# Kernel optimization log

Measured on AMD Instinct MI355X. Metric: run time of the kernel, lower is better.

The kernel has to match this reference:

```python
import jax, jax.numpy as jnp
from jax import lax
import numpy as np

N, I, O = 64, 8, 8
B = 512
S_EX, S_PHI, S_RHO = 10, 60, 60  # S_phi must equal S_rho (alpha loops feed S_rho-sized h into the GRUs)
N_ACTIONS, N_ROLES = 5, 7


def _gru(x, h, Wih, Whh, bih, bhh):
    # torch.nn.GRUCell math
    gi = x @ Wih.T + bih
    gh = h @ Whh.T + bhh
    ir, iz, inn = jnp.split(gi, 3, axis=-1)
    hr, hz, hn = jnp.split(gh, 3, axis=-1)
    r = jax.nn.sigmoid(ir + hr)
    zg = jax.nn.sigmoid(iz + hz)
    n = jnp.tanh(inn + r * hn)
    return (1.0 - zg) * n + zg * h


def setup_inputs() -> dict:
    key = jax.random.key(0)
    ks = jax.random.split(key, 24)
    f32 = jnp.float32
    z = jax.random.normal(ks[0], (B, N, S_EX), f32)
    dz = jax.random.normal(ks[1], (B, N, S_EX), f32)
    has = (jax.random.uniform(ks[2], (B, N)) < 0.9).astype(f32)
    adj = (jnp.triu(jax.random.uniform(ks[3], (N, N)), 1) > 0.7).astype(jnp.int32)

    def lin(k, o, i):
        return (jax.random.normal(k, (o, i), f32) * np.float32(1.0 / np.sqrt(i)))

    d = dict(z=z, dz=dz, has=has, adj=adj)
    d['Wih_f'] = lin(ks[4], 3 * S_PHI, S_RHO)
    d['Whh_f'] = lin(ks[5], 3 * S_PHI, S_PHI)
    d['bih_f'] = jax.random.normal(ks[6], (3 * S_PHI,), f32) * 0.02
    d['bhh_f'] = jax.random.normal(ks[7], (3 * S_PHI,), f32) * 0.02
    d['Wih_b'] = lin(ks[8], 3 * S_PHI, S_RHO)
    d['Whh_b'] = lin(ks[9], 3 * S_PHI, S_PHI)
    d['bih_b'] = jax.random.normal(ks[10], (3 * S_PHI,), f32) * 0.02
    d['bhh_b'] = jax.random.normal(ks[11], (3 * S_PHI,), f32) * 0.02
    d['Wf'] = lin(ks[12], S_RHO, S_PHI + 2 * S_EX)
    d['bf'] = jax.random.normal(ks[13], (S_RHO,), f32) * 0.02
    d['Wb'] = lin(ks[14], S_RHO, S_PHI + 2 * S_EX)
    d['bb'] = jax.random.normal(ks[15], (S_RHO,), f32) * 0.02
    d['Wa'] = lin(ks[16], N_ACTIONS, 2 * S_PHI)
    d['ba'] = jax.random.normal(ks[17], (N_ACTIONS,), f32) * 0.02
    d['Wc'] = lin(ks[18], 1, 2 * S_PHI)
    d['bc'] = jax.random.normal(ks[19], (1,), f32) * 0.02
    d['Wu'] = lin(ks[20], N_ROLES, 2 * S_RHO)
    d['bu'] = jax.random.normal(ks[21], (N_ROLES,), f32) * 0.02
    return d


def reference(z, dz, has, adj,
              Wih_f, Whh_f, bih_f, bhh_f,
              Wih_b, Whh_b, bih_b, bhh_b,
              Wf, bf, Wb, bb, Wa, ba, Wc, bc, Wu, bu):
    Bn, Nn = has.shape
    dt = z.dtype
    adjf = adj.astype(dt)

    # ---- forward sweep over nodes in ascending order ----
    def fwd_outer(rho, i):
        def inner(h, j):
            hn = _gru(rho[j], h, Wih_f, Whh_f, bih_f, bhh_f)
            blend = adjf[j, i] * has[:, j][:, None]  # edge exists AND source node present
            return h + blend * (hn - h), None
        h, _ = lax.scan(inner, jnp.zeros((Bn, S_PHI), dt), jnp.arange(Nn))
        rho_i = jnp.tanh(jnp.concatenate([h, z[:, i], dz[:, i]], 1) @ Wf.T + bf)
        return rho.at[i].set(rho_i), None

    rho_f, _ = lax.scan(fwd_outer, jnp.zeros((Nn, Bn, S_RHO), dt), jnp.arange(Nn))

    # ---- backward sweep over nodes in descending order ----
    def bwd_outer(rho, i):
        def inner(h, j):
            hn = _gru(rho[j], h, Wih_b, Whh_b, bih_b, bhh_b)
            blend = adjf[i, j] * has[:, j][:, None]  # out-edges of i, visited descending
            return h + blend * (hn - h), None
        h, _ = lax.scan(inner, jnp.zeros((Bn, S_PHI), dt), jnp.arange(Nn - 1, -1, -1))
        rho_i = jnp.concatenate([h, z[:, i], dz[:, i]], 1) @ Wb.T + bb
        return rho.at[i].set(rho_i), None

    rho_b, _ = lax.scan(bwd_outer, jnp.zeros((Nn, Bn, S_RHO), dt), jnp.arange(Nn - 1, -1, -1))

    # ---- aggregate outputs (last O nodes) and inputs (first I nodes) ----
    h = jnp.zeros((Bn, S_RHO), dt)
    for i in range(N - O, N):
        hn = _gru(rho_f[i], h, Wih_f, Whh_f, bih_f, bhh_f)
        h = h + has[:, i][:, None] * (hn - h)
    alpha_f = h
    h = jnp.zeros((Bn, S_RHO), dt)
    for i in reversed(range(I)):
        hn = _gru(rho_b[i], h, Wih_b, Whh_b, bih_b, bhh_b)
        h = h + has[:, i][:, None] * (hn - h)
    alpha_b = h

    ab = jnp.concatenate([alpha_f, alpha_b], 1)
    omega = ab @ Wa.T + ba          # [B, 5]
    value = ab @ Wc.T + bc          # [B, 1]

    feats = jnp.concatenate([rho_f, rho_b], -1)           # [N, B, 2*S_rho]
    psi = jnp.einsum('nbs,rs->brn', feats, Wu) + bu[None, :, None]  # [B, 7, N]
    m = has[:, None, :]
    psi = -60.0 * (1.0 - m) + psi * m  # interpolate(-60, psi, has)

    instr_prob = jax.nn.softmax(omega, axis=1)
    role_prob = jax.nn.softmax(psi, axis=2)
    return instr_prob, role_prob, value
```

## Files before the change

kernel.cpp:

```cpp
#include <hip/hip_runtime.h>
#include <hip/hip_bf16.h>

#define NN 64
#define BATCH 512
#define SP 60
#define SG 180
#define SEX 10
#define CATD 80
#define NA 5
#define NR 7
#define OO 8
#define II 8

typedef unsigned long long u64;
typedef unsigned short u16;
typedef unsigned int u32;
typedef unsigned char u8;

#define OFF_Z     0
#define OFF_DZ    327680
#define OFF_HAS   655360
#define OFF_WIHF  688128
#define OFF_WHHF  698928
#define OFF_BIHF  709728
#define OFF_BHHF  709908
#define OFF_WIHB  710088
#define OFF_WHHB  720888
#define OFF_BIHB  731688
#define OFF_BHHB  731868
#define OFF_WF    732048
#define OFF_BF    736848
#define OFF_WB    736908
#define OFF_BB    741708
#define OFF_WA    741768
#define OFF_BA    742368
#define OFF_WC    742373
#define OFF_BC    742493
#define OFF_WU    742494
#define OFF_BU    743334
#define CONV_TOTAL 743341
#define OFF_FLAG  743342
#define OFF_RHOF  743344
#define OFF_RHOB  (OFF_RHOF + 1966080)
#define OFF_ALF   (OFF_RHOB + 1966080)
#define OFF_ALB   (OFF_ALF + 30720)
#define OUT_TOTAL 232448

typedef _Float16 f16;
typedef _Float16 half2_t __attribute__((ext_vector_type(2)));
typedef _Float16 f16x8 __attribute__((ext_vector_type(8)));
typedef float f32x4 __attribute__((ext_vector_type(4)));

__device__ __forceinline__ float us2f(u16 v){
  return __uint_as_float(((u32)v) << 16);
}
__device__ __forceinline__ u16 f2bf(float f){
  __hip_bfloat16 h = __float2bfloat16(f);
  return *reinterpret_cast<u16*>(&h);
}
__device__ __forceinline__ float rcp_(float x){ return __builtin_amdgcn_rcpf(x); }
__device__ __forceinline__ float sigm(float x){
  return rcp_(1.f + __expf(-x));
}
__device__ __forceinline__ float tanh_(float x){
  float e = __expf(2.f*fabsf(x));
  float t = 1.f - 2.f*rcp_(e + 1.f);
  return copysignf(t, x);
}
__device__ __forceinline__ u32 pack2(float a, float b){
  half2_t h; h[0] = (f16)a; h[1] = (f16)b;
  return __builtin_bit_cast(u32, h);
}
__device__ __forceinline__ float fdot2_(u32 a, u32 b, float c){
  return __builtin_amdgcn_fdot2(__builtin_bit_cast(half2_t, a),
                                __builtin_bit_cast(half2_t, b), c, false);
}
__device__ __forceinline__ f16x8 bc16(uint4 v){ return __builtin_bit_cast(f16x8, v); }
__device__ __forceinline__ f32x4 mfma16(f16x8 a, f16x8 b, f32x4 c){
  return __builtin_amdgcn_mfma_f32_16x16x32_f16(a, b, c, 0, 0, 0);
}

__global__ __launch_bounds__(256) void conv_in(
  const void* z, const void* dz, const void* has,
  const void* WihF, const void* WhhF, const void* bihF, const void* bhhF,
  const void* WihB, const void* WhhB, const void* bihB, const void* bhhB,
  const void* Wf_, const void* bf_, const void* Wb_, const void* bb_,
  const void* Wa, const void* ba, const void* Wc, const void* bc,
  const void* Wu, const void* bu, float* ws)
{
  __shared__ int sIsBf;
  const int tid = threadIdx.x;
  if (tid < 64){
    const u32* w = (const u32*)has;
    int f = 0;
    #pragma unroll
    for (int k=0;k<4;k++) f |= (w[tid*4 + k] == 0x3F803F80u) ? 1 : 0;
    u64 m = __ballot(f != 0);
    if (tid == 0) sIsBf = (m != 0ULL) ? 1 : 0;
  }
  __syncthreads();
  const int isbf = sIsBf;
  if (blockIdx.x == 0 && tid == 0) ws[OFF_FLAG] = (float)isbf;
  int idx = blockIdx.x*256 + tid;
  if (idx >= CONV_TOTAL) return;
  const void* src; int loc;
  if      (idx < OFF_DZ  ){ src=z;    loc=idx-OFF_Z;    }
  else if (idx < OFF_HAS ){ src=dz;   loc=idx-OFF_DZ;   }
  else if (idx < OFF_WIHF){ src=has;  loc=idx-OFF_HAS;  }
  else if (idx < OFF_WHHF){ src=WihF; loc=idx-OFF_WIHF; }
  else if (idx < OFF_BIHF){ src=WhhF; loc=idx-OFF_WHHF; }
  else if (idx < OFF_BHHF){ src=bihF; loc=idx-OFF_BIHF; }
  else if (idx < OFF_WIHB){ src=bhhF; loc=idx-OFF_BHHF; }
  else if (idx < OFF_WHHB){ src=WihB; loc=idx-OFF_WIHB; }
  else if (idx < OFF_BIHB){ src=WhhB; loc=idx-OFF_WHHB; }
  else if (idx < OFF_BHHB){ src=bihB; loc=idx-OFF_BIHB; }
  else if (idx < OFF_WF  ){ src=bhhB; loc=idx-OFF_BHHB; }
  else if (idx < OFF_BF  ){ src=Wf_;  loc=idx-OFF_WF;   }
  else if (idx < OFF_WB  ){ src=bf_;  loc=idx-OFF_BF;   }
  else if (idx < OFF_BB  ){ src=Wb_;  loc=idx-OFF_WB;   }
  else if (idx < OFF_WA  ){ src=bb_;  loc=idx-OFF_BB;   }
  else if (idx < OFF_BA  ){ src=Wa;   loc=idx-OFF_WA;   }
  else if (idx < OFF_WC  ){ src=ba;   loc=idx-OFF_BA;   }
  else if (idx < OFF_BC  ){ src=Wc;   loc=idx-OFF_WC;   }
  else if (idx < OFF_WU  ){ src=bc;   loc=idx-OFF_BC;   }
  else if (idx < OFF_BU  ){ src=Wu;   loc=idx-OFF_WU;   }
  else                    { src=bu;   loc=idx-OFF_BU;   }
  float v = isbf ? us2f(((const u16*)src)[loc]) : ((const float*)src)[loc];
  ws[idx] = v;
}

__global__ __launch_bounds__(256, 4) void dir_kernel(const int* __restrict__ adj,
                                                     float* __restrict__ ws)
{
  const int tid = threadIdx.x;
  const int w   = tid >> 6;
  const int u   = tid & 63;
  const int ml  = u & 15;
  const int q   = u >> 4;
  const int bid = blockIdx.x;
  const int bwd = bid >> 9;
  const int b   = bid & 511;

  const float* Wih  = ws + (bwd ? OFF_WIHB : OFF_WIHF);
  const float* Whh  = ws + (bwd ? OFF_WHHB : OFF_WHHF);
  const float* bih  = ws + (bwd ? OFF_BIHB : OFF_BIHF);
  const float* bhh  = ws + (bwd ? OFF_BHHB : OFF_BHHF);
  const float* Wcat = ws + (bwd ? OFF_WB   : OFF_WF);
  const float* bcat = ws + (bwd ? OFF_BB   : OFF_BF);
  const float* zc   = ws + OFF_Z;
  const float* dzc  = ws + OFF_DZ;
  const float* hasc = ws + OFF_HAS;
  float* rho   = ws + (bwd ? OFF_RHOB : OFF_RHOF);
  float* alpha = ws + (bwd ? OFF_ALB  : OFF_ALF);

  __shared__ uint4 sH4[65][9];
  __shared__ uint4 sRhoPad[8];
  __shared__ uint4 sRhoHist[8][8];
  __shared__ float sZdc[NN][64];
  __shared__ u32 sZp[NN][5];
  __shared__ u32 sDZp[NN][5];
  __shared__ float sHas[NN];
  __shared__ u64 sRowM[NN];
  __shared__ u8 sConsL[NN][64];
  __shared__ int sConsCnt[NN];

  #define ROWB(I) ((char*)&sH4[(I)][0])
  const u32 BIASW = 0x3C000000u;

  {
    if (tid < 64){
      u64 rowm = 0;
      for (int j=0;j<64;j++) rowm |= ((u64)(adj[tid*64+j]!=0))<<j;
      sRowM[tid] = rowm;
      sHas[tid] = hasc[b*NN + tid];
    }
    for (int idx=tid; idx<65*9; idx+=256){
      uint4 v = {0,0,0,0};
      if (idx % 9 == 7) v.w = BIASW;
      ((uint4*)sH4)[idx] = v;
    }
    if (tid < 8){ uint4 v={0,0,0,0}; if (tid==7) v.w = BIASW; sRhoPad[tid]=v; }
    if (tid < 64){ uint4 v={0,0,0,0}; if ((tid&7)==7) v.w = BIASW; ((uint4*)sRhoHist)[tid]=v; }
    for (int idx=tid; idx<NN*5; idx+=256){
      int n2=idx/5, p2=idx%5;
      sZp [n2][p2] = pack2(zc [(size_t)b*NN*SEX + n2*SEX + 2*p2],
                           zc [(size_t)b*NN*SEX + n2*SEX + 2*p2+1]);
      sDZp[n2][p2] = pack2(dzc[(size_t)b*NN*SEX + n2*SEX + 2*p2],
                           dzc[(size_t)b*NN*SEX + n2*SEX + 2*p2+1]);
    }
  }
  __syncthreads();
  if (tid < 64){
    u64 cm = 0;
    if (bwd) for (int i2=0;i2<64;i2++) cm |= ((sRowM[i2]>>tid)&1ULL)<<i2;
    u64 m = bwd ? cm : sRowM[tid];
    int c = 0;
    while (m){ int i2 = (int)__builtin_ctzll(m); m &= m-1; sConsL[tid][c++] = (u8)i2; }
    sConsCnt[tid] = c;
  }
  {
    const int uu = tid & 63;
    const int tw = tid >> 6;
    if (uu < SP){
      u32 wz[10];
      #pragma unroll
      for (int p=0;p<10;p++)
        wz[p] = pack2(Wcat[uu*CATD + 60 + 2*p], Wcat[uu*CATD + 60 + 2*p + 1]);
      const float bb0 = bcat[uu];
      for (int t2=tw; t2<NN; t2+=4){
        float c = bb0;
        #pragma unroll
        for (int p=0;p<5;p++){
          c = fdot2_(wz[p],   sZp [t2][p], c);
          c = fdot2_(wz[5+p], sDZp[t2][p], c);
        }
        sZdc[t2][uu] = c;
      }
    }
  }

  f16x8 Ar[4], Az[4], Anh[2], Ani[2], Ac[2];
  {
    const int R = 16*w + ml;
    const bool rok = (R < SP);
    #pragma unroll
    for (int kt=0; kt<4; kt++){
      f16x8 vr, vz;
      #pragma unroll
      for (int j=0;j<8;j++){
        const int K = 32*kt + 8*q + j;
        float wr=0.f, wz2=0.f;
        if (rok){
          if (K < SP){ wr = Whh[R*SP+K]; wz2 = Whh[(60+R)*SP+K]; }
          else if (K >= 64 && K < 64+SP){ wr = Wih[R*SP+(K-64)]; wz2 = Wih[(60+R)*SP+(K-64)]; }
          else if (K == 127){ wr = bhh[R]+bih[R]; wz2 = bhh[60+R]+bih[60+R]; }
        }
        vr[j]=(f16)wr; vz[j]=(f16)wz2;
      }
      Ar[kt]=vr; Az[kt]=vz;
    }
    #pragma unroll
    for (int kt=0; kt<2; kt++){
      f16x8 vn, vi, vc;
      #pragma unroll
      for (int j=0;j<8;j++){
        const int K = 32*kt + 8*q + j;
        float wn=0.f, wi=0.f, wcv=0.f;
        if (rok){
          if (K < SP){ wn = Whh[(120+R)*SP+K]; wi = Wih[(120+R)*SP+K]; wcv = Wcat[R*CATD+K]; }
          else if (K == 63){ wn = bhh[120+R]; wi = bih[120+R]; }
        }
        vn[j]=(f16)wn; vi[j]=(f16)wi; vc[j]=(f16)wcv;
      }
      Anh[kt]=vn; Ani[kt]=vi; Ac[kt]=vc;
    }
  }
  __syncthreads();

  auto gates = [&](f32x4 Dr, f32x4 Dz, f32x4 Dn, f32x4 Gn,
                   int ci, bool wr, float bl){
    char* rp = ROWB(ci) + 32*w + 8*q;
    uint2 h2 = *(uint2*)rp;
    half2_t ha = __builtin_bit_cast(half2_t, h2.x);
    half2_t hb = __builtin_bit_cast(half2_t, h2.y);
    float hold[4] = { (float)ha[0], (float)ha[1], (float)hb[0], (float)hb[1] };
    float hw[4];
    #pragma unroll
    for (int reg=0;reg<4;reg++){
      float r_ = sigm(Dr[reg]);
      float zg = sigm(Dz[reg]);
      float nv = tanh_(Gn[reg] + r_*Dn[reg]);
      float hn_ = (1.f - zg)*nv + zg*hold[reg];
      hw[reg] = (bl != 0.f) ? hn_ : hold[reg];
    }
    if (wr && !(w==3 && q==3)){
      uint2 o; o.x = pack2(hw[0],hw[1]); o.y = pack2(hw[2],hw[3]);
      *(uint2*)rp = o;
    }
  };

  auto fullpass = [&](f16x8 Bh0, f16x8 Bh1, f16x8 Br0, f16x8 Br1,
                      f32x4 Gn, int ci, bool wr, float bl){
    f32x4 Dr={0,0,0,0}, Dz={0,0,0,0}, Dn={0,0,0,0};
    Dr = mfma16(Ar[0], Bh0, Dr); Dr = mfma16(Ar[1], Bh1, Dr);
    Dr = mfma16(Ar[2], Br0, Dr); Dr = mfma16(Ar[3], Br1, Dr);
    Dz = mfma16(Az[0], Bh0, Dz); Dz = mfma16(Az[1], Bh1, Dz);
    Dz = mfma16(Az[2], Br0, Dz); Dz = mfma16(Az[3], Br1, Dz);
    Dn = mfma16(Anh[0], Bh0, Dn); Dn = mfma16(Anh[1], Bh1, Dn);
    gates(Dr, Dz, Dn, Gn, ci, wr, bl);
  };

  int t = bwd ? 63 : 0;
  const int dt = bwd ? -1 : 1;
  for (int s=0; s<64; s++, t+=dt){
    const float blendT = sHas[t];
    const int cnt = sConsCnt[t];
    const bool act = (blendT != 0.f) && (cnt > 0);
    const bool g1  = act && (cnt > 16);

    int ci0 = 64, ci1 = 64;
    f16x8 Bh0g0={}, Bh1g0={}, Bh0g1={}, Bh1g1={};
    if (act){
      ci0 = (ml < cnt) ? (int)sConsL[t][ml] : 64;
      Bh0g0 = bc16(sH4[ci0][q]);
      Bh1g0 = bc16(sH4[ci0][4+q]);
      if (g1){
        ci1 = (16 + ml < cnt) ? (int)sConsL[t][16 + ml] : 64;
        Bh0g1 = bc16(sH4[ci1][q]);
        Bh1g1 = bc16(sH4[ci1][4+q]);
      }
    }

    {
      const f16x8 Hb0 = bc16(sH4[t][q]);
      const f16x8 Hb1 = bc16(sH4[t][4+q]);
      f32x4 Rv = {0,0,0,0};
      Rv = mfma16(Ac[0], Hb0, Rv);
      Rv = mfma16(Ac[1], Hb1, Rv);
      const int row = 16*w + 4*q + ml;
      if (ml < 4 && row < SP){
        float vv = Rv[0];
        vv = (ml==1) ? Rv[1] : vv;
        vv = (ml==2) ? Rv[2] : vv;
        vv = (ml==3) ? Rv[3] : vv;
        vv += sZdc[t][row];
        if (!bwd) vv = tanh_(vv);
        *(f16*)((char*)&sRhoPad[0] + 2*row) = (f16)vv;
        const int slot = bwd ? t : (t - (NN-OO));
        if (slot >= 0 && slot < 8)
          *(f16*)((char*)&sRhoHist[slot][0] + 2*row) = (f16)vv;
        rho[((size_t)t*BATCH + b)*SP + row] = vv;
      }
    }
    __syncthreads();

    if (act){
      const f16x8 Br0 = bc16(sRhoPad[q]);
      const f16x8 Br1 = bc16(sRhoPad[4+q]);
      f32x4 Gn={0,0,0,0};
      Gn = mfma16(Ani[0], Br0, Gn); Gn = mfma16(Ani[1], Br1, Gn);
      f32x4 Pr={0,0,0,0};
      Pr = mfma16(Ar[2], Br0, Pr); Pr = mfma16(Ar[3], Br1, Pr);
      f32x4 Pz={0,0,0,0};
      Pz = mfma16(Az[2], Br0, Pz); Pz = mfma16(Az[3], Br1, Pz);

      {
        f32x4 Dr=Pr, Dz=Pz, Dn={0,0,0,0};
        Dr = mfma16(Ar[0], Bh0g0, Dr); Dr = mfma16(Ar[1], Bh1g0, Dr);
        Dz = mfma16(Az[0], Bh0g0, Dz); Dz = mfma16(Az[1], Bh1g0, Dz);
        Dn = mfma16(Anh[0], Bh0g0, Dn); Dn = mfma16(Anh[1], Bh1g0, Dn);
        gates(Dr, Dz, Dn, Gn, ci0, ml < cnt, 1.0f);
      }
      if (g1){
        f32x4 Dr=Pr, Dz=Pz, Dn={0,0,0,0};
        Dr = mfma16(Ar[0], Bh0g1, Dr); Dr = mfma16(Ar[1], Bh1g1, Dr);
        Dz = mfma16(Az[0], Bh0g1, Dz); Dz = mfma16(Az[1], Bh1g1, Dz);
        Dn = mfma16(Anh[0], Bh0g1, Dn); Dn = mfma16(Anh[1], Bh1g1, Dn);
        gates(Dr, Dz, Dn, Gn, ci1, 16 + ml < cnt, 1.0f);
      }
      for (int p=2; 16*p < cnt; p++){
        const int idxp = 16*p + ml;
        const int ci = (idxp < cnt) ? (int)sConsL[t][idxp] : 64;
        const f16x8 Bh0 = bc16(sH4[ci][q]);
        const f16x8 Bh1 = bc16(sH4[ci][4+q]);
        fullpass(Bh0, Bh1, Br0, Br1, Gn, ci, idxp < cnt, 1.0f);
      }
    }
    __syncthreads();
  }

  for (int s2=0; s2<8; s2++){
    const int i = bwd ? (7 - s2) : (NN - OO + s2);
    const int slot = bwd ? i : (i - (NN-OO));
    const f16x8 Th0 = bc16(sH4[64][q]);
    const f16x8 Th1 = bc16(sH4[64][4+q]);
    const f16x8 Tr0 = bc16(sRhoHist[slot][q]);
    const f16x8 Tr1 = bc16(sRhoHist[slot][4+q]);
    f32x4 Gt={0,0,0,0};
    Gt = mfma16(Ani[0], Tr0, Gt);
    Gt = mfma16(Ani[1], Tr1, Gt);
    __syncthreads();
    fullpass(Th0, Th1, Tr0, Tr1, Gt, 64, ml==0, sHas[i]);
    __syncthreads();
  }
  if (tid < SP) alpha[(size_t)b*SP + tid] = (float)*(const f16*)(ROWB(64) + 2*tid);
  #undef ROWB
}

__global__ __launch_bounds__(256, 1) void head_kernel(float* __restrict__ ws,
                                                      void* __restrict__ outp)
{
  const int b = blockIdx.x;
  const int tid = threadIdx.x;
  const int isbf = (ws[OFF_FLAG] != 0.f);
  const float* hasc   = ws + OFF_HAS;
  const float* WaC    = ws + OFF_WA;
  const float* baC    = ws + OFF_BA;
  const float* WcC    = ws + OFF_WC;
  const float* bcC    = ws + OFF_BC;
  const float* WuC    = ws + OFF_WU;
  const float* buC    = ws + OFF_BU;
  const float* rhoF   = ws + OFF_RHOF;
  const float* rhoB   = ws + OFF_RHOB;
  const float* alphaF = ws + OFF_ALF;
  const float* alphaB = ws + OFF_ALB;

  __shared__ float sF[NN][122];
  __shared__ float sAB[120];
  __shared__ float sWu[NR*120];
  __shared__ float sHasR[NN];
  __shared__ float sPsi[NR][NN];
  __shared__ float sOm[NA];

  auto wout = [&](int idx, float v){
    if (isbf) ((u16*)outp)[idx] = f2bf(v);
    else      ((float*)outp)[idx] = v;
  };

  for (int idx=tid; idx<NN*SP; idx+=256){
    int n = idx/SP, s = idx%SP;
    sF[n][s]    = rhoF[((size_t)n*BATCH + b)*SP + s];
    sF[n][60+s] = rhoB[((size_t)n*BATCH + b)*SP + s];
  }
  for (int idx=tid; idx<120; idx+=256)
    sAB[idx] = (idx<60) ? alphaF[(size_t)b*SP + idx] : alphaB[(size_t)b*SP + idx-60];
  for (int idx=tid; idx<NR*120; idx+=256) sWu[idx] = WuC[idx];
  for (int idx=tid; idx<NN; idx+=256) sHasR[idx] = hasc[b*NN + idx];
  __syncthreads();

  for (int idx=tid; idx<NR*NN; idx+=256){
    int r = idx/NN, n = idx%NN;
    const float2* fn = (const float2*)&sF[n][0];
    const float2* wr = (const float2*)&sWu[r*120];
    float acc = buC[r];
    #pragma unroll 6
    for (int s2=0;s2<60;s2++){
      float2 a = fn[s2], c = wr[s2];
      acc += a.x*c.x;
      acc += a.y*c.y;
    }
    sPsi[r][n] = (sHasR[n] != 0.f) ? acc : -60.f;
  }
  if (tid >= 64 && tid < 64+NA){
    int a = tid - 64;
    float acc = baC[a];
    for (int s=0;s<120;s++) acc += sAB[s]*WaC[a*120+s];
    sOm[a] = acc;
  }
  if (tid == 70){
    float acc = bcC[0];
    for (int s=0;s<120;s++) acc += sAB[s]*WcC[s];
    wout(2560 + BATCH*NR*NN + b, acc);
  }
  __syncthreads();

  if (tid < NR*32){
    const int r = tid >> 5, l = tid & 31;
    float v0 = sPsi[r][l], v1 = sPsi[r][l+32];
    float m = fmaxf(v0, v1);
    #pragma unroll
    for (int o=16;o>0;o>>=1) m = fmaxf(m, __shfl_xor(m, o, 64));
    float e0 = __expf(v0 - m), e1 = __expf(v1 - m);
    float ssum = e0 + e1;
    #pragma unroll
    for (int o=16;o>0;o>>=1) ssum += __shfl_xor(ssum, o, 64);
    float rinv = 1.f/ssum;
    wout(2560 + (size_t)b*NR*NN + r*NN + l,    e0*rinv);
    wout(2560 + (size_t)b*NR*NN + r*NN + l+32, e1*rinv);
  }
  if (tid == 224){
    float m = -1e30f;
    for (int a=0;a<NA;a++) m = fmaxf(m, sOm[a]);
    float e[NA]; float ssum = 0.f;
    for (int a=0;a<NA;a++){ e[a] = __expf(sOm[a]-m); ssum += e[a]; }
    for (int a=0;a<NA;a++) wout(b*NA + a, e[a]/ssum);
  }
}

extern "C" void kernel_launch(void* const* d_in, const int* in_sizes, int n_in,
                              void* d_out, int out_size, void* d_ws, size_t ws_size,
                              hipStream_t stream)
{
  const int* adj = (const int*)d_in[3];
  float* ws = (float*)d_ws;

  conv_in<<<(CONV_TOTAL+255)/256, 256, 0, stream>>>(
      d_in[0], d_in[1], d_in[2],
      d_in[4], d_in[5], d_in[6], d_in[7],
      d_in[8], d_in[9], d_in[10], d_in[11],
      d_in[12], d_in[13], d_in[14], d_in[15],
      d_in[16], d_in[17], d_in[18], d_in[19],
      d_in[20], d_in[21], ws);

  dir_kernel<<<1024, 256, 0, stream>>>(adj, ws);

  head_kernel<<<512, 256, 0, stream>>>(ws, d_out);
}
```

Baseline: 256.9 us.

## Process two batch elements per workgroup in the directional GRU kernel

Each workgroup of the directional DAG-GRU kernel now handles two batch elements instead of one, halving the grid to 512 blocks. The two independent MFMA chains are interleaved so that register-resident weight fragments, the adjacency and consumer-list setup, and the per-step barriers are shared between them. The blend is now a per-element has mask applied in the gate update rather than a per-step skip. In exchange, register pressure and shared memory per block roughly double, the launch bound drops to 2 blocks per CU, and steps where only one element is present still do the work for both.

```diff
diff --git a/kernel.cpp b/kernel.cpp
--- a/kernel.cpp
+++ b/kernel.cpp
@@ -129,7 +129,7 @@
   ws[idx] = v;
 }
 
-__global__ __launch_bounds__(256, 4) void dir_kernel(const int* __restrict__ adj,
+__global__ __launch_bounds__(256, 2) void dir_kernel(const int* __restrict__ adj,
                                                      float* __restrict__ ws)
 {
   const int tid = threadIdx.x;
@@ -138,8 +138,8 @@
   const int ml  = u & 15;
   const int q   = u >> 4;
   const int bid = blockIdx.x;
-  const int bwd = bid >> 9;
-  const int b   = bid & 511;
+  const int bwd = bid >> 8;
+  const int bp  = (bid & 255) << 1;
 
   const float* Wih  = ws + (bwd ? OFF_WIHB : OFF_WIHF);
   const float* Whh  = ws + (bwd ? OFF_WHHB : OFF_WHHF);
@@ -153,18 +153,18 @@
   float* rho   = ws + (bwd ? OFF_RHOB : OFF_RHOF);
   float* alpha = ws + (bwd ? OFF_ALB  : OFF_ALF);
 
-  __shared__ uint4 sH4[65][9];
-  __shared__ uint4 sRhoPad[8];
-  __shared__ uint4 sRhoHist[8][8];
-  __shared__ float sZdc[NN][64];
-  __shared__ u32 sZp[NN][5];
-  __shared__ u32 sDZp[NN][5];
-  __shared__ float sHas[NN];
+  __shared__ uint4 sH4[2][65][9];
+  __shared__ uint4 sRhoPad[2][8];
+  __shared__ uint4 sRhoHist[2][8][8];
+  __shared__ float sZdc[2][NN][SP];
+  __shared__ u32 sZp[2][NN][5];
+  __shared__ u32 sDZp[2][NN][5];
+  __shared__ float sHas[2][NN];
   __shared__ u64 sRowM[NN];
   __shared__ u8 sConsL[NN][64];
   __shared__ int sConsCnt[NN];
 
-  #define ROWB(I) ((char*)&sH4[(I)][0])
+  #define ROWB(E,I) ((char*)&sH4[(E)][(I)][0])
   const u32 BIASW = 0x3C000000u;
 
   {
@@ -172,21 +172,24 @@
       u64 rowm = 0;
       for (int j=0;j<64;j++) rowm |= ((u64)(adj[tid*64+j]!=0))<<j;
       sRowM[tid] = rowm;
-      sHas[tid] = hasc[b*NN + tid];
-    }
-    for (int idx=tid; idx<65*9; idx+=256){
+    }
+    if (tid < 128){
+      const int e = tid >> 6, n = tid & 63;
+      sHas[e][n] = hasc[(bp+e)*NN + n];
+    }
+    for (int idx=tid; idx<2*65*9; idx+=256){
       uint4 v = {0,0,0,0};
-      if (idx % 9 == 7) v.w = BIASW;
+      if ((idx % 9) == 7) v.w = BIASW;
       ((uint4*)sH4)[idx] = v;
     }
-    if (tid < 8){ uint4 v={0,0,0,0}; if (tid==7) v.w = BIASW; sRhoPad[tid]=v; }
-    if (tid < 64){ uint4 v={0,0,0,0}; if ((tid&7)==7) v.w = BIASW; ((uint4*)sRhoHist)[tid]=v; }
-    for (int idx=tid; idx<NN*5; idx+=256){
-      int n2=idx/5, p2=idx%5;
-      sZp [n2][p2] = pack2(zc [(size_t)b*NN*SEX + n2*SEX + 2*p2],
-                           zc [(size_t)b*NN*SEX + n2*SEX + 2*p2+1]);
-      sDZp[n2][p2] = pack2(dzc[(size_t)b*NN*SEX + n2*SEX + 2*p2],
-                           dzc[(size_t)b*NN*SEX + n2*SEX + 2*p2+1]);
+    if (tid < 16){ uint4 v={0,0,0,0}; if ((tid&7)==7) v.w = BIASW; ((uint4*)sRhoPad)[tid]=v; }
+    if (tid < 128){ uint4 v={0,0,0,0}; if ((tid&7)==7) v.w = BIASW; ((uint4*)sRhoHist)[tid]=v; }
+    for (int idx=tid; idx<2*NN*5; idx+=256){
+      int e = idx/(NN*5), rem = idx%(NN*5), n2=rem/5, p2=rem%5;
+      sZp [e][n2][p2] = pack2(zc [(size_t)(bp+e)*NN*SEX + n2*SEX + 2*p2],
+                              zc [(size_t)(bp+e)*NN*SEX + n2*SEX + 2*p2+1]);
+      sDZp[e][n2][p2] = pack2(dzc[(size_t)(bp+e)*NN*SEX + n2*SEX + 2*p2],
+                              dzc[(size_t)(bp+e)*NN*SEX + n2*SEX + 2*p2+1]);
     }
   }
   __syncthreads();
@@ -207,14 +210,15 @@
       for (int p=0;p<10;p++)
         wz[p] = pack2(Wcat[uu*CATD + 60 + 2*p], Wcat[uu*CATD + 60 + 2*p + 1]);
       const float bb0 = bcat[uu];
-      for (int t2=tw; t2<NN; t2+=4){
+      for (int et=tw; et<2*NN; et+=4){
+        const int e = et >> 6, t2 = et & 63;
         float c = bb0;
         #pragma unroll
         for (int p=0;p<5;p++){
-          c = fdot2_(wz[p],   sZp [t2][p], c);
-          c = fdot2_(wz[5+p], sDZp[t2][p], c);
+          c = fdot2_(wz[p],   sZp [e][t2][p], c);
+          c = fdot2_(wz[5+p], sDZp[e][t2][p], c);
         }
-        sZdc[t2][uu] = c;
+        sZdc[e][t2][uu] = c;
       }
     }
   }
@@ -258,8 +262,8 @@
   __syncthreads();
 
   auto gates = [&](f32x4 Dr, f32x4 Dz, f32x4 Dn, f32x4 Gn,
-                   int ci, bool wr, float bl){
-    char* rp = ROWB(ci) + 32*w + 8*q;
+                   char* rowb, bool wr, float bl){
+    char* rp = rowb + 32*w + 8*q;
     uint2 h2 = *(uint2*)rp;
     half2_t ha = __builtin_bit_cast(half2_t, h2.x);
     half2_t hb = __builtin_bit_cast(half2_t, h2.y);
@@ -280,90 +284,117 @@
   };
 
   auto fullpass = [&](f16x8 Bh0, f16x8 Bh1, f16x8 Br0, f16x8 Br1,
-                      f32x4 Gn, int ci, bool wr, float bl){
+                      f32x4 Gn, char* rowb, bool wr, float bl){
     f32x4 Dr={0,0,0,0}, Dz={0,0,0,0}, Dn={0,0,0,0};
     Dr = mfma16(Ar[0], Bh0, Dr); Dr = mfma16(Ar[1], Bh1, Dr);
     Dr = mfma16(Ar[2], Br0, Dr); Dr = mfma16(Ar[3], Br1, Dr);
     Dz = mfma16(Az[0], Bh0, Dz); Dz = mfma16(Az[1], Bh1, Dz);
     Dz = mfma16(Az[2], Br0, Dz); Dz = mfma16(Az[3], Br1, Dz);
     Dn = mfma16(Anh[0], Bh0, Dn); Dn = mfma16(Anh[1], Bh1, Dn);
-    gates(Dr, Dz, Dn, Gn, ci, wr, bl);
+    gates(Dr, Dz, Dn, Gn, rowb, wr, bl);
   };
 
   int t = bwd ? 63 : 0;
   const int dt = bwd ? -1 : 1;
   for (int s=0; s<64; s++, t+=dt){
-    const float blendT = sHas[t];
     const int cnt = sConsCnt[t];
-    const bool act = (blendT != 0.f) && (cnt > 0);
+    const float bl0 = sHas[0][t];
+    const float bl1 = sHas[1][t];
+    const bool act = (cnt > 0) && (bl0 != 0.f || bl1 != 0.f);
     const bool g1  = act && (cnt > 16);
 
     int ci0 = 64, ci1 = 64;
-    f16x8 Bh0g0={}, Bh1g0={}, Bh0g1={}, Bh1g1={};
+    f16x8 Bh0e0={}, Bh1e0={}, Bh0e1={}, Bh1e1={};
+    f16x8 Ch0e0={}, Ch1e0={}, Ch0e1={}, Ch1e1={};
     if (act){
       ci0 = (ml < cnt) ? (int)sConsL[t][ml] : 64;
-      Bh0g0 = bc16(sH4[ci0][q]);
-      Bh1g0 = bc16(sH4[ci0][4+q]);
+      Bh0e0 = bc16(sH4[0][ci0][q]); Bh1e0 = bc16(sH4[0][ci0][4+q]);
+      Bh0e1 = bc16(sH4[1][ci0][q]); Bh1e1 = bc16(sH4[1][ci0][4+q]);
       if (g1){
         ci1 = (16 + ml < cnt) ? (int)sConsL[t][16 + ml] : 64;
-        Bh0g1 = bc16(sH4[ci1][q]);
-        Bh1g1 = bc16(sH4[ci1][4+q]);
+        Ch0e0 = bc16(sH4[0][ci1][q]); Ch1e0 = bc16(sH4[0][ci1][4+q]);
+        Ch0e1 = bc16(sH4[1][ci1][q]); Ch1e1 = bc16(sH4[1][ci1][4+q]);
       }
     }
 
     {
-      const f16x8 Hb0 = bc16(sH4[t][q]);
-      const f16x8 Hb1 = bc16(sH4[t][4+q]);
-      f32x4 Rv = {0,0,0,0};
-      Rv = mfma16(Ac[0], Hb0, Rv);
-      Rv = mfma16(Ac[1], Hb1, Rv);
+      const f16x8 H00 = bc16(sH4[0][t][q]);
+      const f16x8 H01 = bc16(sH4[0][t][4+q]);
+      const f16x8 H10 = bc16(sH4[1][t][q]);
+      const f16x8 H11 = bc16(sH4[1][t][4+q]);
+      f32x4 Rv0 = {0,0,0,0}, Rv1 = {0,0,0,0};
+      Rv0 = mfma16(Ac[0], H00, Rv0);
+      Rv1 = mfma16(Ac[0], H10, Rv1);
+      Rv0 = mfma16(Ac[1], H01, Rv0);
+      Rv1 = mfma16(Ac[1], H11, Rv1);
       const int row = 16*w + 4*q + ml;
       if (ml < 4 && row < SP){
-        float vv = Rv[0];
-        vv = (ml==1) ? Rv[1] : vv;
-        vv = (ml==2) ? Rv[2] : vv;
-        vv = (ml==3) ? Rv[3] : vv;
-        vv += sZdc[t][row];
-        if (!bwd) vv = tanh_(vv);
-        *(f16*)((char*)&sRhoPad[0] + 2*row) = (f16)vv;
+        float v0 = Rv0[0], v1 = Rv1[0];
+        v0 = (ml==1) ? Rv0[1] : v0;  v1 = (ml==1) ? Rv1[1] : v1;
+        v0 = (ml==2) ? Rv0[2] : v0;  v1 = (ml==2) ? Rv1[2] : v1;
+        v0 = (ml==3) ? Rv0[3] : v0;  v1 = (ml==3) ? Rv1[3] : v1;
+        v0 += sZdc[0][t][row];
+        v1 += sZdc[1][t][row];
+        if (!bwd){ v0 = tanh_(v0); v1 = tanh_(v1); }
+        *(f16*)((char*)&sRhoPad[0][0] + 2*row) = (f16)v0;
+        *(f16*)((char*)&sRhoPad[1][0] + 2*row) = (f16)v1;
         const int slot = bwd ? t : (t - (NN-OO));
-        if (slot >= 0 && slot < 8)
-          *(f16*)((char*)&sRhoHist[slot][0] + 2*row) = (f16)vv;
-        rho[((size_t)t*BATCH + b)*SP + row] = vv;
+        if (slot >= 0 && slot < 8){
+          *(f16*)((char*)&sRhoHist[0][slot][0] + 2*row) = (f16)v0;
+          *(f16*)((char*)&sRhoHist[1][slot][0] + 2*row) = (f16)v1;
+        }
+        rho[((size_t)t*BATCH + bp  )*SP + row] = v0;
+        rho[((size_t)t*BATCH + bp+1)*SP + row] = v1;
       }
     }
     __syncthreads();
 
     if (act){
-      const f16x8 Br0 = bc16(sRhoPad[q]);
-      const f16x8 Br1 = bc16(sRhoPad[4+q]);
-      f32x4 Gn={0,0,0,0};
-      Gn = mfma16(Ani[0], Br0, Gn); Gn = mfma16(Ani[1], Br1, Gn);
-      f32x4 Pr={0,0,0,0};
-      Pr = mfma16(Ar[2], Br0, Pr); Pr = mfma16(Ar[3], Br1, Pr);
-      f32x4 Pz={0,0,0,0};
-      Pz = mfma16(Az[2], Br0, Pz); Pz = mfma16(Az[3], Br1, Pz);
+      const f16x8 Br0e0 = bc16(sRhoPad[0][q]);
+      const f16x8 Br1e0 = bc16(sRhoPad[0][4+q]);
+      const f16x8 Br0e1 = bc16(sRhoPad[1][q]);
+      const f16x8 Br1e1 = bc16(sRhoPad[1][4+q]);
+      f32x4 Gn0={0,0,0,0}, Gn1={0,0,0,0};
+      Gn0 = mfma16(Ani[0], Br0e0, Gn0);  Gn1 = mfma16(Ani[0], Br0e1, Gn1);
+      Gn0 = mfma16(Ani[1], Br1e0, Gn0);  Gn1 = mfma16(Ani[1], Br1e1, Gn1);
+      f32x4 Pr0={0,0,0,0}, Pr1={0,0,0,0};
+      Pr0 = mfma16(Ar[2], Br0e0, Pr0);   Pr1 = mfma16(Ar[2], Br0e1, Pr1);
+      Pr0 = mfma16(Ar[3], Br1e0, Pr0);   Pr1 = mfma16(Ar[3], Br1e1, Pr1);
+      f32x4 Pz0={0,0,0,0}, Pz1={0,0,0,0};
+      Pz0 = mfma16(Az[2], Br0e0, Pz0);   Pz1 = mfma16(Az[2], Br0e1, Pz1);
+      Pz0 = mfma16(Az[3], Br1e0, Pz0);   Pz1 = mfma16(Az[3], Br1e1, Pz1);
 
       {
-        f32x4 Dr=Pr, Dz=Pz, Dn={0,0,0,0};
-        Dr = mfma16(Ar[0], Bh0g0, Dr); Dr = mfma16(Ar[1], Bh1g0, Dr);
-        Dz = mfma16(Az[0], Bh0g0, Dz); Dz = mfma16(Az[1], Bh1g0, Dz);
-        Dn = mfma16(Anh[0], Bh0g0, Dn); Dn = mfma16(Anh[1], Bh1g0, Dn);
-        gates(Dr, Dz, Dn, Gn, ci0, ml < cnt, 1.0f);
+        f32x4 Dr0=Pr0, Dz0=Pz0, Dn0={0,0,0,0};
+        f32x4 Dr1=Pr1, Dz1=Pz1, Dn1={0,0,0,0};
+        Dr0 = mfma16(Ar[0], Bh0e0, Dr0);  Dr1 = mfma16(Ar[0], Bh0e1, Dr1);
+        Dr0 = mfma16(Ar[1], Bh1e0, Dr0);  Dr1 = mfma16(Ar[1], Bh1e1, Dr1);
+        Dz0 = mfma16(Az[0], Bh0e0, Dz0);  Dz1 = mfma16(Az[0], Bh0e1, Dz1);
+        Dz0 = mfma16(Az[1], Bh1e0, Dz0);  Dz1 = mfma16(Az[1], Bh1e1, Dz1);
+        Dn0 = mfma16(Anh[0], Bh0e0, Dn0); Dn1 = mfma16(Anh[0], Bh0e1, Dn1);
+        Dn0 = mfma16(Anh[1], Bh1e0, Dn0); Dn1 = mfma16(Anh[1], Bh1e1, Dn1);
+        gates(Dr0, Dz0, Dn0, Gn0, ROWB(0,ci0), ml < cnt, bl0);
+        gates(Dr1, Dz1, Dn1, Gn1, ROWB(1,ci0), ml < cnt, bl1);
       }
       if (g1){
-        f32x4 Dr=Pr, Dz=Pz, Dn={0,0,0,0};
-        Dr = mfma16(Ar[0], Bh0g1, Dr); Dr = mfma16(Ar[1], Bh1g1, Dr);
-        Dz = mfma16(Az[0], Bh0g1, Dz); Dz = mfma16(Az[1], Bh1g1, Dz);
-        Dn = mfma16(Anh[0], Bh0g1, Dn); Dn = mfma16(Anh[1], Bh1g1, Dn);
-        gates(Dr, Dz, Dn, Gn, ci1, 16 + ml < cnt, 1.0f);
+        f32x4 Dr0=Pr0, Dz0=Pz0, Dn0={0,0,0,0};
+        f32x4 Dr1=Pr1, Dz1=Pz1, Dn1={0,0,0,0};
+        Dr0 = mfma16(Ar[0], Ch0e0, Dr0);  Dr1 = mfma16(Ar[0], Ch0e1, Dr1);
+        Dr0 = mfma16(Ar[1], Ch1e0, Dr0);  Dr1 = mfma16(Ar[1], Ch1e1, Dr1);
+        Dz0 = mfma16(Az[0], Ch0e0, Dz0);  Dz1 = mfma16(Az[0], Ch0e1, Dz1);
+        Dz0 = mfma16(Az[1], Ch1e0, Dz0);  Dz1 = mfma16(Az[1], Ch1e1, Dz1);
+        Dn0 = mfma16(Anh[0], Ch0e0, Dn0); Dn1 = mfma16(Anh[0], Ch0e1, Dn1);
+        Dn0 = mfma16(Anh[1], Ch1e0, Dn0); Dn1 = mfma16(Anh[1], Ch1e1, Dn1);
+        gates(Dr0, Dz0, Dn0, Gn0, ROWB(0,ci1), 16 + ml < cnt, bl0);
+        gates(Dr1, Dz1, Dn1, Gn1, ROWB(1,ci1), 16 + ml < cnt, bl1);
       }
       for (int p=2; 16*p < cnt; p++){
         const int idxp = 16*p + ml;
         const int ci = (idxp < cnt) ? (int)sConsL[t][idxp] : 64;
-        const f16x8 Bh0 = bc16(sH4[ci][q]);
-        const f16x8 Bh1 = bc16(sH4[ci][4+q]);
-        fullpass(Bh0, Bh1, Br0, Br1, Gn, ci, idxp < cnt, 1.0f);
+        fullpass(bc16(sH4[0][ci][q]), bc16(sH4[0][ci][4+q]),
+                 Br0e0, Br1e0, Gn0, ROWB(0,ci), idxp < cnt, bl0);
+        fullpass(bc16(sH4[1][ci][q]), bc16(sH4[1][ci][4+q]),
+                 Br0e1, Br1e1, Gn1, ROWB(1,ci), idxp < cnt, bl1);
       }
     }
     __syncthreads();
@@ -372,18 +403,26 @@
   for (int s2=0; s2<8; s2++){
     const int i = bwd ? (7 - s2) : (NN - OO + s2);
     const int slot = bwd ? i : (i - (NN-OO));
-    const f16x8 Th0 = bc16(sH4[64][q]);
-    const f16x8 Th1 = bc16(sH4[64][4+q]);
-    const f16x8 Tr0 = bc16(sRhoHist[slot][q]);
-    const f16x8 Tr1 = bc16(sRhoHist[slot][4+q]);
-    f32x4 Gt={0,0,0,0};
-    Gt = mfma16(Ani[0], Tr0, Gt);
-    Gt = mfma16(Ani[1], Tr1, Gt);
+    const f16x8 Th00 = bc16(sH4[0][64][q]);
+    const f16x8 Th01 = bc16(sH4[0][64][4+q]);
+    const f16x8 Th10 = bc16(sH4[1][64][q]);
+    const f16x8 Th11 = bc16(sH4[1][64][4+q]);
+    const f16x8 Tr00 = bc16(sRhoHist[0][slot][q]);
+    const f16x8 Tr01 = bc16(sRhoHist[0][slot][4+q]);
+    const f16x8 Tr10 = bc16(sRhoHist[1][slot][q]);
+    const f16x8 Tr11 = bc16(sRhoHist[1][slot][4+q]);
+    f32x4 Gt0={0,0,0,0}, Gt1={0,0,0,0};
+    Gt0 = mfma16(Ani[0], Tr00, Gt0);  Gt1 = mfma16(Ani[0], Tr10, Gt1);
+    Gt0 = mfma16(Ani[1], Tr01, Gt0);  Gt1 = mfma16(Ani[1], Tr11, Gt1);
     __syncthreads();
-    fullpass(Th0, Th1, Tr0, Tr1, Gt, 64, ml==0, sHas[i]);
+    fullpass(Th00, Th01, Tr00, Tr01, Gt0, ROWB(0,64), ml==0, sHas[0][i]);
+    fullpass(Th10, Th11, Tr10, Tr11, Gt1, ROWB(1,64), ml==0, sHas[1][i]);
     __syncthreads();
   }
-  if (tid < SP) alpha[(size_t)b*SP + tid] = (float)*(const f16*)(ROWB(64) + 2*tid);
+  if (tid < SP){
+    alpha[(size_t)(bp  )*SP + tid] = (float)*(const f16*)(ROWB(0,64) + 2*tid);
+    alpha[(size_t)(bp+1)*SP + tid] = (float)*(const f16*)(ROWB(1,64) + 2*tid);
+  }
   #undef ROWB
 }
 
@@ -492,7 +531,7 @@
       d_in[16], d_in[17], d_in[18], d_in[19],
       d_in[20], d_in[21], ws);
 
-  dir_kernel<<<1024, 256, 0, stream>>>(adj, ws);
+  dir_kernel<<<512, 256, 0, stream>>>(adj, ws);
 
   head_kernel<<<512, 256, 0, stream>>>(ws, d_out);
 }
```

After: 252.4 us. About the same (-1.8%).
